# Optimization experiments

Measured on AMD Instinct MI355X. Metric: run time of the kernel, lower is better.

Reference implementation:

```python
import jax, jax.numpy as jnp
import numpy as np

N = 100000      # nodes
E = 1600000     # edges (avg degree 16)
IN = 256
OUT = 128
H = 8
DK = OUT // H   # 16
SQRT_DK = float(np.sqrt(DK))


def setup_inputs() -> dict:
    key = jax.random.key(0)
    ks = jax.random.split(key, 16)

    def w(k, i, o):
        return jax.random.normal(k, (i, o), jnp.float32) * (1.0 / np.sqrt(i))

    def b(k, o):
        return jax.random.normal(k, (o,), jnp.float32) * 0.01

    return {
        "h": jax.random.normal(ks[0], (N, IN), jnp.float32),
        "Wq": w(ks[1], IN, OUT), "bq": b(ks[2], OUT),
        "Wk": w(ks[3], IN, OUT), "bk": b(ks[4], OUT),
        "Wv": w(ks[5], IN, OUT), "bv": b(ks[6], OUT),
        "Wmsg": w(ks[7], OUT, OUT), "bmsg": b(ks[8], OUT),
        "Wattn": w(ks[9], OUT, OUT), "battn": b(ks[10], OUT),
        "Wa": w(ks[11], OUT, OUT), "ba": b(ks[12], OUT),
        "src": jax.random.randint(ks[13], (E,), 0, N, dtype=jnp.int32),
        "dst": jax.random.randint(ks[14], (E,), 0, N, dtype=jnp.int32),
    }


def reference(h, Wq, bq, Wk, bk, Wv, bv, Wmsg, bmsg, Wattn, battn, Wa, ba, src, dst):
    # node projections: [N, H, DK]
    k = ((h @ Wk + bk) @ Wattn + battn).reshape(N, H, DK)
    v = ((h @ Wv + bv) @ Wmsg + bmsg).reshape(N, H, DK)
    q = (h @ Wq + bq).reshape(N, H, DK)

    # SDDMM: per-edge dot product k[src] . q[dst], per head -> [E, H]
    s = jnp.einsum('ehd,ehd->eh', k[src], q[dst]) / SQRT_DK

    # edge softmax, normalized over incoming edges of each dst node
    m = jax.ops.segment_max(s, dst, num_segments=N)      # [N, H]
    e = jnp.exp(s - m[dst])                              # [E, H]
    z = jax.ops.segment_sum(e, dst, num_segments=N)      # [N, H]
    attn = e / z[dst]                                    # [E, H]

    # SPMM: weighted aggregation of v[src] into dst -> [N, H, DK]
    msg = v[src] * attn[:, :, None]
    agg = jax.ops.segment_sum(msg, dst, num_segments=N).reshape(N, OUT)

    return agg @ Wa + ba
```

## Files before the change

kernel.cpp:

```cpp
#include <hip/hip_runtime.h>
#include <hip/hip_fp16.h>

#define IN_F 256
#define OUT_F 128
#define QKV_F 384
#define HEADS 8
#define DKH 16

typedef _Float16 f16x8 __attribute__((ext_vector_type(8)));
typedef float    f32x4 __attribute__((ext_vector_type(4)));

__global__ void prep_W(const float* __restrict__ Wq,
                       const float* __restrict__ Wk, const float* __restrict__ Wattn,
                       const float* __restrict__ Wv, const float* __restrict__ Wmsg,
                       _Float16* __restrict__ WT_all) {
    int k = blockIdx.x;
    int c = threadIdx.x;
    float r;
    if (c < 128) {
        r = Wq[k * 128 + c];
    } else if (c < 256) {
        int cc = c - 128;
        float s = 0.f;
        for (int j = 0; j < 128; ++j) s += Wk[k * 128 + j] * Wattn[j * 128 + cc];
        r = s;
    } else {
        int cc = c - 256;
        float s = 0.f;
        for (int j = 0; j < 128; ++j) s += Wv[k * 128 + j] * Wmsg[j * 128 + cc];
        r = s;
    }
    WT_all[(size_t)c * IN_F + k] = (_Float16)r;
}

__global__ void prep_b(const float* __restrict__ bq, const float* __restrict__ bk,
                       const float* __restrict__ battn, const float* __restrict__ bv,
                       const float* __restrict__ bmsg, const float* __restrict__ Wattn,
                       const float* __restrict__ Wmsg, float* __restrict__ b_all) {
    int c = threadIdx.x;
    float r;
    if (c < 128) {
        r = bq[c];
    } else if (c < 256) {
        int cc = c - 128;
        float s = battn[cc];
        for (int j = 0; j < 128; ++j) s += bk[j] * Wattn[j * 128 + cc];
        r = s;
    } else {
        int cc = c - 256;
        float s = bmsg[cc];
        for (int j = 0; j < 128; ++j) s += bv[j] * Wmsg[j * 128 + cc];
        r = s;
    }
    b_all[c] = r;
}

__global__ void t_cast16(const float* __restrict__ W, _Float16* __restrict__ WT,
                         int K, int N) {
    int k = blockIdx.x;
    int c = threadIdx.x;
    WT[(size_t)c * K + k] = (_Float16)W[(size_t)k * N + c];
}

template<int KD, int ND, bool QKV_EPI>
__global__ __launch_bounds__(256) void mfma_gemm(
        const float* __restrict__ A, const _Float16* __restrict__ BT,
        const float* __restrict__ bias, float* __restrict__ Cq,
        __half* __restrict__ kv16, int M) {
    constexpr int BMR  = 64;
    constexpr int NT_W = ND / 64;
    __shared__ __align__(16) _Float16 As[BMR * KD];

    int t   = threadIdx.x;
    int wv  = t >> 6;
    int L   = t & 63;
    int row0 = blockIdx.x * BMR;

    {
        int r   = t >> 2;
        int sub = t & 3;
        int gr  = row0 + r;
        const float* Ap = A + (size_t)gr * KD;
        bool val = gr < M;
#pragma unroll
        for (int i = 0; i < KD / 32; ++i) {
            int k0 = (sub + 4 * i) * 8;
            float4 x0 = make_float4(0.f, 0.f, 0.f, 0.f), x1 = x0;
            if (val) {
                x0 = *(const float4*)(Ap + k0);
                x1 = *(const float4*)(Ap + k0 + 4);
            }
            f16x8 hv;
            hv[0] = (_Float16)x0.x; hv[1] = (_Float16)x0.y;
            hv[2] = (_Float16)x0.z; hv[3] = (_Float16)x0.w;
            hv[4] = (_Float16)x1.x; hv[5] = (_Float16)x1.y;
            hv[6] = (_Float16)x1.z; hv[7] = (_Float16)x1.w;
            int ks = k0 ^ (8 * (r & 7));
            *(f16x8*)&As[r * KD + ks] = hv;
        }
    }
    __syncthreads();

    int colbase = wv * (ND / 4);
    int rL = L & 15;
    int kL = (L >> 4) * 8;

    f32x4 acc[4][NT_W] = {};
#pragma unroll
    for (int ks = 0; ks < KD; ks += 32) {
        f16x8 af[4];
#pragma unroll
        for (int mt = 0; mt < 4; ++mt) {
            int r = mt * 16 + rL;
            int k = (ks + kL) ^ (8 * (r & 7));
            af[mt] = *(const f16x8*)&As[r * KD + k];
        }
#pragma unroll
        for (int nt = 0; nt < NT_W; ++nt) {
            f16x8 bf = *(const f16x8*)(BT + (size_t)(colbase + nt * 16 + rL) * KD
                                       + ks + kL);
#pragma unroll
            for (int mt = 0; mt < 4; ++mt)
                acc[mt][nt] = __builtin_amdgcn_mfma_f32_16x16x32_f16(
                    af[mt], bf, acc[mt][nt], 0, 0, 0);
        }
    }

    int cr0 = (L >> 4) * 4;
    int cc  = L & 15;
#pragma unroll
    for (int nt = 0; nt < NT_W; ++nt) {
        int col = colbase + nt * 16 + cc;
        float b = bias[col];
#pragma unroll
        for (int mt = 0; mt < 4; ++mt) {
#pragma unroll
            for (int j = 0; j < 4; ++j) {
                int R = row0 + mt * 16 + cr0 + j;
                if (R < M) {
                    float v = acc[mt][nt][j] + b;
                    if (QKV_EPI) {
                        if (col < 128) Cq[(size_t)R * 128 + col] = v;
                        else kv16[(size_t)R * 256 + (col - 128)] = __float2half(v);
                    } else {
                        Cq[(size_t)R * ND + col] = v;
                    }
                }
            }
        }
    }
}

__global__ void k_hist(const int* __restrict__ dst, int* __restrict__ deg, int e) {
    int i = blockIdx.x * 256 + threadIdx.x;
    if (i < e) atomicAdd(&deg[dst[i]], 1);
}

__global__ void k_scan1(const int* __restrict__ in, int* __restrict__ out,
                        int* __restrict__ bsums, int n) {
    __shared__ int sc[256];
    int t = threadIdx.x;
    int base = blockIdx.x * 1024 + t * 4;
    int v[4];
#pragma unroll
    for (int i = 0; i < 4; ++i) v[i] = (base + i < n) ? in[base + i] : 0;
    int tsum = v[0] + v[1] + v[2] + v[3];
    sc[t] = tsum;
    __syncthreads();
    for (int off = 1; off < 256; off <<= 1) {
        int x = 0;
        if (t >= off) x = sc[t - off];
        __syncthreads();
        sc[t] += x;
        __syncthreads();
    }
    int incl = sc[t];
    int e = incl - tsum;
#pragma unroll
    for (int i = 0; i < 4; ++i) {
        if (base + i < n) out[base + i] = e;
        e += v[i];
    }
    if (t == 255) bsums[blockIdx.x] = incl;
}

__global__ void k_scan2(int* __restrict__ bsums, int nb) {
    __shared__ int sc[256];
    int t = threadIdx.x;
    int v = (t < nb) ? bsums[t] : 0;
    sc[t] = v;
    __syncthreads();
    for (int off = 1; off < 256; off <<= 1) {
        int x = 0;
        if (t >= off) x = sc[t - off];
        __syncthreads();
        sc[t] += x;
        __syncthreads();
    }
    if (t < nb) bsums[t] = sc[t] - v;
}

__global__ void k_scan3(int* __restrict__ out, const int* __restrict__ bsums, int n) {
    int i = blockIdx.x * 256 + threadIdx.x;
    if (i < n) out[i] += bsums[blockIdx.x >> 2];
}

__global__ void k_scatter(const int* __restrict__ src, const int* __restrict__ dst,
                          const int* __restrict__ row_start, int* __restrict__ cursor,
                          int* __restrict__ sorted_src, int e) {
    int i = blockIdx.x * 256 + threadIdx.x;
    if (i < e) {
        int d  = dst[i];
        int p  = atomicAdd(&cursor[d], 1);
        sorted_src[row_start[d] + p] = src[i];
    }
}

__global__ __launch_bounds__(256) void edge_agg(
        const float* __restrict__ qbuf, const __half* __restrict__ kv16,
        const int* __restrict__ row_start, const int* __restrict__ deg,
        const int* __restrict__ sorted_src,
        float* __restrict__ agg, int nnodes) {
    int wid  = threadIdx.x >> 6;
    int lane = threadIdx.x & 63;
    int node = blockIdx.x * 4 + wid;
    if (node >= nnodes) return;

    const float2 qv = *(const float2*)(qbuf + (size_t)node * 128 + 2 * lane);
    float m = -INFINITY, z = 0.f, acc0 = 0.f, acc1 = 0.f;
    int rs = row_start[node];
    int dg = deg[node];

    for (int base = 0; base < dg; base += 16) {
        int rem = dg - base;
        int my_src = (lane < 16 && base + lane < dg) ? sorted_src[rs + base + lane] : 0;

        unsigned int kbits[16], vbits[16];
#pragma unroll
        for (int j = 0; j < 16; ++j) {
            int sn = __builtin_amdgcn_readlane(my_src, j);
            const __half* rowp = kv16 + (size_t)sn * 256 + 2 * lane;
            kbits[j] = *(const unsigned int*)rowp;
            vbits[j] = *(const unsigned int*)(rowp + 128);
        }

        float s[16];
#pragma unroll
        for (int j = 0; j < 16; ++j) {
            float2 kf = __half22float2(*(const __half2*)&kbits[j]);
            float pp = kf.x * qv.x + kf.y * qv.y;
            pp += __shfl_xor(pp, 1);
            pp += __shfl_xor(pp, 2);
            pp += __shfl_xor(pp, 4);
            s[j] = (j < rem) ? pp * 0.25f : -INFINITY;
        }

        float cm = s[0];
#pragma unroll
        for (int j = 1; j < 16; ++j) cm = fmaxf(cm, s[j]);
        float mn = fmaxf(m, cm);
        float f  = __expf(m - mn);
        acc0 *= f; acc1 *= f;
        float zc = 0.f;
#pragma unroll
        for (int j = 0; j < 16; ++j) {
            float w = __expf(s[j] - mn);
            zc += w;
            float2 vf = __half22float2(*(const __half2*)&vbits[j]);
            acc0 = fmaf(w, vf.x, acc0);
            acc1 = fmaf(w, vf.y, acc1);
        }
        z = z * f + zc;
        m = mn;
    }
    float inv = (z > 0.f) ? 1.f / z : 0.f;
    *(float2*)(agg + (size_t)node * OUT_F + 2 * lane) =
        make_float2(acc0 * inv, acc1 * inv);
}

extern "C" void kernel_launch(void* const* d_in, const int* in_sizes, int n_in,
                              void* d_out, int out_size, void* d_ws, size_t ws_size,
                              hipStream_t stream) {
    const float* h     = (const float*)d_in[0];
    const float* Wq    = (const float*)d_in[1];
    const float* bq    = (const float*)d_in[2];
    const float* Wk    = (const float*)d_in[3];
    const float* bk    = (const float*)d_in[4];
    const float* Wv    = (const float*)d_in[5];
    const float* bv    = (const float*)d_in[6];
    const float* Wmsg  = (const float*)d_in[7];
    const float* bmsg  = (const float*)d_in[8];
    const float* Wattn = (const float*)d_in[9];
    const float* battn = (const float*)d_in[10];
    const float* Wa    = (const float*)d_in[11];
    const float* ba    = (const float*)d_in[12];
    const int*   src   = (const int*)d_in[13];
    const int*   dst   = (const int*)d_in[14];
    float* out = (float*)d_out;

    int nn = in_sizes[0] / IN_F;
    int ne = in_sizes[13];

    char* p = (char*)d_ws;
    auto carve = [&](size_t bytes) {
        char* r = p;
        p += (bytes + 255) & ~(size_t)255;
        return r;
    };
    _Float16* WT_all = (_Float16*)carve((size_t)QKV_F * IN_F * 2);
    _Float16* WaT    = (_Float16*)carve((size_t)OUT_F * OUT_F * 2);
    float*    b_all  = (float*)carve((size_t)QKV_F * 4);
    float*    qbuf   = (float*)carve((size_t)nn * 128 * 4);
    __half*   kv16   = (__half*)carve((size_t)nn * 256 * 2);
    float*    agg    = (float*)carve((size_t)nn * OUT_F * 4);
    int* deg     = (int*)carve((size_t)nn * 4);
    int* rowst   = (int*)carve((size_t)nn * 4);
    int* cursor  = (int*)carve((size_t)nn * 4);
    int* bsums   = (int*)carve(4096);
    int* ssrc    = (int*)carve((size_t)ne * 4);

    hipMemsetAsync(deg, 0, (size_t)nn * 4, stream);
    hipMemsetAsync(cursor, 0, (size_t)nn * 4, stream);

    prep_W<<<IN_F, QKV_F, 0, stream>>>(Wq, Wk, Wattn, Wv, Wmsg, WT_all);
    prep_b<<<1, QKV_F, 0, stream>>>(bq, bk, battn, bv, bmsg, Wattn, Wmsg, b_all);
    t_cast16<<<OUT_F, OUT_F, 0, stream>>>(Wa, WaT, OUT_F, OUT_F);

    mfma_gemm<IN_F, QKV_F, true><<<(nn + 63) / 64, 256, 0, stream>>>(
        h, WT_all, b_all, qbuf, kv16, nn);

    k_hist<<<(ne + 255) / 256, 256, 0, stream>>>(dst, deg, ne);
    int nb = (nn + 1023) / 1024;
    k_scan1<<<nb, 256, 0, stream>>>(deg, rowst, bsums, nn);
    k_scan2<<<1, 256, 0, stream>>>(bsums, nb);
    k_scan3<<<(nn + 255) / 256, 256, 0, stream>>>(rowst, bsums, nn);
    k_scatter<<<(ne + 255) / 256, 256, 0, stream>>>(src, dst, rowst, cursor, ssrc, ne);

    edge_agg<<<(nn + 3) / 4, 256, 0, stream>>>(qbuf, kv16, rowst, deg, ssrc, agg, nn);

    mfma_gemm<OUT_F, OUT_F, false><<<(nn + 63) / 64, 256, 0, stream>>>(
        agg, WaT, ba, out, nullptr, nn);
}
```

Before: 610.0 us.

## Make MFMA GEMMs persistent with register-resident B tiles and column-split grid

The projection GEMMs become persistent kernels: each block holds a fixed 128-column slice of the transposed weights in registers and loops over row tiles with a grid-stride. The QKV GEMM is split across three column blocks via blockIdx.y, so each block computes only 128 output columns. This removes the repeated global loads of B fragments for every row tile. In exchange, the activation rows of the QKV GEMM are loaded and converted three times, once per column block, and a second barrier is added per tile.

```diff
diff --git a/kernel.cpp b/kernel.cpp
--- a/kernel.cpp
+++ b/kernel.cpp
@@ -62,91 +62,100 @@
     WT[(size_t)c * K + k] = (_Float16)W[(size_t)k * N + c];
 }
 
-template<int KD, int ND, bool QKV_EPI>
+template<int KD, bool QKV_EPI>
 __global__ __launch_bounds__(256) void mfma_gemm(
         const float* __restrict__ A, const _Float16* __restrict__ BT,
         const float* __restrict__ bias, float* __restrict__ Cq,
-        __half* __restrict__ kv16, int M) {
-    constexpr int BMR  = 64;
-    constexpr int NT_W = ND / 64;
-    __shared__ __align__(16) _Float16 As[BMR * KD];
-
-    int t   = threadIdx.x;
-    int wv  = t >> 6;
-    int L   = t & 63;
-    int row0 = blockIdx.x * BMR;
-
-    {
-        int r   = t >> 2;
-        int sub = t & 3;
-        int gr  = row0 + r;
-        const float* Ap = A + (size_t)gr * KD;
-        bool val = gr < M;
-#pragma unroll
-        for (int i = 0; i < KD / 32; ++i) {
-            int k0 = (sub + 4 * i) * 8;
-            float4 x0 = make_float4(0.f, 0.f, 0.f, 0.f), x1 = x0;
-            if (val) {
-                x0 = *(const float4*)(Ap + k0);
-                x1 = *(const float4*)(Ap + k0 + 4);
-            }
-            f16x8 hv;
-            hv[0] = (_Float16)x0.x; hv[1] = (_Float16)x0.y;
-            hv[2] = (_Float16)x0.z; hv[3] = (_Float16)x0.w;
-            hv[4] = (_Float16)x1.x; hv[5] = (_Float16)x1.y;
-            hv[6] = (_Float16)x1.z; hv[7] = (_Float16)x1.w;
-            int ks = k0 ^ (8 * (r & 7));
-            *(f16x8*)&As[r * KD + ks] = hv;
-        }
-    }
-    __syncthreads();
-
-    int colbase = wv * (ND / 4);
+        __half* __restrict__ kv16, int M, int ntiles, int nrowblk) {
+    constexpr int NKQ = KD / 32;
+    __shared__ __align__(16) _Float16 As[64 * KD];
+
+    int t  = threadIdx.x;
+    int wv = t >> 6;
+    int L  = t & 63;
     int rL = L & 15;
     int kL = (L >> 4) * 8;
-
-    f32x4 acc[4][NT_W] = {};
-#pragma unroll
-    for (int ks = 0; ks < KD; ks += 32) {
-        f16x8 af[4];
-#pragma unroll
-        for (int mt = 0; mt < 4; ++mt) {
-            int r = mt * 16 + rL;
-            int k = (ks + kL) ^ (8 * (r & 7));
-            af[mt] = *(const f16x8*)&As[r * KD + k];
-        }
-#pragma unroll
-        for (int nt = 0; nt < NT_W; ++nt) {
-            f16x8 bf = *(const f16x8*)(BT + (size_t)(colbase + nt * 16 + rL) * KD
-                                       + ks + kL);
+    int colbase = blockIdx.y * 128 + wv * 32;
+
+    f16x8 Breg[2][NKQ];
+#pragma unroll
+    for (int nt = 0; nt < 2; ++nt)
+#pragma unroll
+        for (int kq = 0; kq < NKQ; ++kq)
+            Breg[nt][kq] = *(const f16x8*)(
+                BT + (size_t)(colbase + nt * 16 + rL) * KD + kq * 32 + kL);
+
+    float bb[2] = { bias[colbase + rL], bias[colbase + 16 + rL] };
+
+    int r_  = t >> 2;
+    int sub = t & 3;
+
+    for (int rt = blockIdx.x; rt < ntiles; rt += nrowblk) {
+        int row0 = rt * 64;
+
+        {
+            int gr = row0 + r_;
+            const float* Ap = A + (size_t)gr * KD;
+            bool val = gr < M;
+#pragma unroll
+            for (int i = 0; i < NKQ; ++i) {
+                int k0 = (sub + 4 * i) * 8;
+                float4 x0 = make_float4(0.f, 0.f, 0.f, 0.f), x1 = x0;
+                if (val) {
+                    x0 = *(const float4*)(Ap + k0);
+                    x1 = *(const float4*)(Ap + k0 + 4);
+                }
+                f16x8 hv;
+                hv[0] = (_Float16)x0.x; hv[1] = (_Float16)x0.y;
+                hv[2] = (_Float16)x0.z; hv[3] = (_Float16)x0.w;
+                hv[4] = (_Float16)x1.x; hv[5] = (_Float16)x1.y;
+                hv[6] = (_Float16)x1.z; hv[7] = (_Float16)x1.w;
+                int ks = k0 ^ (8 * (r_ & 7));
+                *(f16x8*)&As[r_ * KD + ks] = hv;
+            }
+        }
+        __syncthreads();
+
+        f32x4 acc[4][2] = {};
+#pragma unroll
+        for (int kq = 0; kq < NKQ; ++kq) {
+            int ksk = kq * 32 + kL;
+            f16x8 af[4];
+#pragma unroll
+            for (int mt = 0; mt < 4; ++mt) {
+                int r = mt * 16 + rL;
+                int k = ksk ^ (8 * (r & 7));
+                af[mt] = *(const f16x8*)&As[r * KD + k];
+            }
+#pragma unroll
+            for (int mt = 0; mt < 4; ++mt) {
+                acc[mt][0] = __builtin_amdgcn_mfma_f32_16x16x32_f16(
+                    af[mt], Breg[0][kq], acc[mt][0], 0, 0, 0);
+                acc[mt][1] = __builtin_amdgcn_mfma_f32_16x16x32_f16(
+                    af[mt], Breg[1][kq], acc[mt][1], 0, 0, 0);
+            }
+        }
+        __syncthreads();
+
+        int cr0 = (L >> 4) * 4;
+#pragma unroll
+        for (int nt = 0; nt < 2; ++nt) {
+            int col = colbase + nt * 16 + rL;
 #pragma unroll
             for (int mt = 0; mt < 4; ++mt)
-                acc[mt][nt] = __builtin_amdgcn_mfma_f32_16x16x32_f16(
-                    af[mt], bf, acc[mt][nt], 0, 0, 0);
-        }
-    }
-
-    int cr0 = (L >> 4) * 4;
-    int cc  = L & 15;
-#pragma unroll
-    for (int nt = 0; nt < NT_W; ++nt) {
-        int col = colbase + nt * 16 + cc;
-        float b = bias[col];
-#pragma unroll
-        for (int mt = 0; mt < 4; ++mt) {
-#pragma unroll
-            for (int j = 0; j < 4; ++j) {
-                int R = row0 + mt * 16 + cr0 + j;
-                if (R < M) {
-                    float v = acc[mt][nt][j] + b;
-                    if (QKV_EPI) {
-                        if (col < 128) Cq[(size_t)R * 128 + col] = v;
-                        else kv16[(size_t)R * 256 + (col - 128)] = __float2half(v);
-                    } else {
-                        Cq[(size_t)R * ND + col] = v;
+#pragma unroll
+                for (int j = 0; j < 4; ++j) {
+                    int R = row0 + mt * 16 + cr0 + j;
+                    if (R < M) {
+                        float v = acc[mt][nt][j] + bb[nt];
+                        if (QKV_EPI) {
+                            if (col < 128) Cq[(size_t)R * 128 + col] = v;
+                            else kv16[(size_t)R * 256 + (col - 128)] = __float2half(v);
+                        } else {
+                            Cq[(size_t)R * 128 + col] = v;
+                        }
                     }
                 }
-            }
         }
     }
 }
@@ -326,8 +335,13 @@
     prep_b<<<1, QKV_F, 0, stream>>>(bq, bk, battn, bv, bmsg, Wattn, Wmsg, b_all);
     t_cast16<<<OUT_F, OUT_F, 0, stream>>>(Wa, WaT, OUT_F, OUT_F);
 
-    mfma_gemm<IN_F, QKV_F, true><<<(nn + 63) / 64, 256, 0, stream>>>(
-        h, WT_all, b_all, qbuf, kv16, nn);
+    int ntiles = (nn + 63) / 64;
+
+    {
+        int nrb = ntiles < 176 ? ntiles : 176;
+        mfma_gemm<IN_F, true><<<dim3(nrb, QKV_F / 128), 256, 0, stream>>>(
+            h, WT_all, b_all, qbuf, kv16, nn, ntiles, nrb);
+    }
 
     k_hist<<<(ne + 255) / 256, 256, 0, stream>>>(dst, deg, ne);
     int nb = (nn + 1023) / 1024;
@@ -338,6 +352,9 @@
 
     edge_agg<<<(nn + 3) / 4, 256, 0, stream>>>(qbuf, kv16, rowst, deg, ssrc, agg, nn);
 
-    mfma_gemm<OUT_F, OUT_F, false><<<(nn + 63) / 64, 256, 0, stream>>>(
-        agg, WaT, ba, out, nullptr, nn);
-}
+    {
+        int nrb = ntiles < 512 ? ntiles : 512;
+        mfma_gemm<OUT_F, false><<<dim3(nrb, 1), 256, 0, stream>>>(
+            agg, WaT, ba, out, nullptr, nn, ntiles, nrb);
+    }
+}
```

New measurement: 568.8 us. 1.07x faster.
